# Kernel optimization log

Hardware: AMD Instinct MI355X
Metric: run time of the kernel (lower is better)

The kernel has to match this reference:

```python
import jax, jax.numpy as jnp
import numpy as np

A, OBS, TD, H, M, ACT, AE = 1024, 2048, 256, 128, 16, 256, 64


def setup_inputs() -> dict:
    key = jax.random.key(0)
    ks = jax.random.split(key, 16)
    p = lambda k, shape: jax.random.normal(k, shape, dtype=jnp.float32) * 0.02
    obs = jax.random.normal(ks[0], (A, OBS), dtype=jnp.float32)
    # group membership matrix: exactly M members per initiator row (ATOC top-m groups)
    scores = jax.random.uniform(ks[1], (A, A))
    idx = jnp.argsort(scores, axis=1)[:, :M]
    C = jnp.zeros((A, A), dtype=bool).at[jnp.arange(A)[:, None], idx].set(True)
    inp = dict(obs=obs, C=C)
    # actor_1: Linear(OBS,TD) -> LN -> ReLU -> Linear(TD,TD) -> LN
    inp['W1'] = p(ks[2], (OBS, TD)); inp['b1'] = jnp.zeros((TD,), jnp.float32)
    inp['g1'] = jnp.ones((TD,), jnp.float32); inp['bt1'] = jnp.zeros((TD,), jnp.float32)
    inp['W2'] = p(ks[3], (TD, TD)); inp['b2'] = jnp.zeros((TD,), jnp.float32)
    inp['g2'] = jnp.ones((TD,), jnp.float32); inp['bt2'] = jnp.zeros((TD,), jnp.float32)
    # attention unit: 2-layer MLP + sigmoid head
    inp['aW1'] = p(ks[4], (TD, AE)); inp['ab1'] = jnp.zeros((AE,), jnp.float32)
    inp['aW2'] = p(ks[5], (AE, AE)); inp['ab2'] = jnp.zeros((AE,), jnp.float32)
    inp['aW3'] = p(ks[6], (AE, 1)); inp['ab3'] = jnp.zeros((1,), jnp.float32)
    # bi-directional LSTM (PyTorch layout: W_ih [4H,TD], W_hh [4H,H])
    inp['Wih_f'] = p(ks[7], (4 * H, TD)); inp['Whh_f'] = p(ks[8], (4 * H, H))
    inp['bih_f'] = jnp.zeros((4 * H,), jnp.float32); inp['bhh_f'] = jnp.zeros((4 * H,), jnp.float32)
    inp['Wih_r'] = p(ks[9], (4 * H, TD)); inp['Whh_r'] = p(ks[10], (4 * H, H))
    inp['bih_r'] = jnp.zeros((4 * H,), jnp.float32); inp['bhh_r'] = jnp.zeros((4 * H,), jnp.float32)
    # actor_2: ReLU -> Linear(TD,TD) -> LN -> Linear(TD,ACT) -> LN -> Tanh
    inp['W3'] = p(ks[11], (TD, TD)); inp['b3'] = jnp.zeros((TD,), jnp.float32)
    inp['g3'] = jnp.ones((TD,), jnp.float32); inp['bt3'] = jnp.zeros((TD,), jnp.float32)
    inp['W4'] = p(ks[12], (TD, ACT)); inp['b4'] = jnp.zeros((ACT,), jnp.float32)
    inp['g4'] = jnp.ones((ACT,), jnp.float32); inp['bt4'] = jnp.zeros((ACT,), jnp.float32)
    return inp


def _ln(x, g, b, eps=1e-5):
    m = jnp.mean(x, -1, keepdims=True)
    v = jnp.mean((x - m) ** 2, -1, keepdims=True)
    return (x - m) * jax.lax.rsqrt(v + eps) * g + b


def _lstm(seq, Wih, Whh, bih, bhh):
    # seq [T, D] -> hidden outputs [T, H]; PyTorch gate order i, f, g, o
    def step(carry, x):
        h, c = carry
        z = x @ Wih.T + bih + h @ Whh.T + bhh
        i, f, g, o = jnp.split(z, 4)
        c = jax.nn.sigmoid(f) * c + jax.nn.sigmoid(i) * jnp.tanh(g)
        h = jax.nn.sigmoid(o) * jnp.tanh(c)
        return (h, c), h
    h0 = jnp.zeros((H,), seq.dtype)
    _, hs = jax.lax.scan(step, (h0, h0), seq)
    return hs


def _forward(obs, C, W1, b1, g1, bt1, W2, b2, g2, bt2, aW1, ab1, aW2, ab2, aW3, ab3,
             Wih_f, Whh_f, bih_f, bhh_f, Wih_r, Whh_r, bih_r, bhh_r,
             W3, b3, g3, bt3, W4, b4, g4, bt4):
    # actor_1
    t = jax.nn.relu(_ln(obs @ W1 + b1, g1, bt1))
    thoughts = _ln(t @ W2 + b2, g2, bt2)  # [A, TD]
    # attention unit -> initiators (threshold 0.5)
    a = jax.nn.relu(thoughts @ aW1 + ab1)
    a = jax.nn.relu(a @ aW2 + ab2)
    init_prob = jax.nn.sigmoid(a @ aW3 + ab3)[:, 0]
    is_init = init_prob > 0.5  # [A]
    tpos = jnp.arange(M)

    def comm_step(th, xs):
        mask, active = xs
        # members first (stable, increasing agent index), padded gather of size M
        order = jnp.argsort((~mask).astype(jnp.int32))[:M]
        gcnt = jnp.sum(mask).astype(jnp.int32)
        seq_f = th[order]                        # [M, TD]
        rev = jnp.clip(gcnt - 1 - tpos, 0, M - 1)
        seq_b = seq_f[rev]                       # valid prefix reversed
        out_f = _lstm(seq_f, Wih_f, Whh_f, bih_f, bhh_f)
        out_b = _lstm(seq_b, Wih_r, Whh_r, bih_r, bhh_r)
        out = jnp.concatenate([out_f, out_b[rev]], axis=-1)  # [M, TD] bi-LSTM aligned
        valid = (tpos < gcnt) & active
        newv = jnp.where(valid[:, None], out, seq_f)         # merge = replace by integrated
        return th.at[order].set(newv), None

    thoughts, _ = jax.lax.scan(comm_step, thoughts, (C, is_init))
    # actor_2
    h = jax.nn.relu(thoughts)
    h = _ln(h @ W3 + b3, g3, bt3)
    acts = jnp.tanh(_ln(h @ W4 + b4, g4, bt4))
    return acts


def reference(obs, C, W1, b1, g1, bt1, W2, b2, g2, bt2, aW1, ab1, aW2, ab2, aW3, ab3,
              Wih_f, Whh_f, bih_f, bhh_f, Wih_r, Whh_r, bih_r, bhh_r,
              W3, b3, g3, bt3, W4, b4, g4, bt4):
    return _forward(obs, C, W1, b1, g1, bt1, W2, b2, g2, bt2, aW1, ab1, aW2, ab2, aW3, ab3,
                    Wih_f, Whh_f, bih_f, bhh_f, Wih_r, Whh_r, bih_r, bhh_r,
                    W3, b3, g3, bt3, W4, b4, g4, bt4)
```

## Files before the change

### kernel.cpp

```cpp
#include <hip/hip_runtime.h>
#include <cstdint>
#include <cstddef>
#include <math.h>

#define A_N   1024
#define OBS_N 2048
#define TD_N  256
#define H_N   128
#define M_N   16
#define AE_N  64
#define NWGC  32

typedef _Float16 h2 __attribute__((ext_vector_type(2)));
typedef _Float16 f16x8 __attribute__((ext_vector_type(8)));
typedef float f32x4 __attribute__((ext_vector_type(4)));

__device__ __forceinline__ float sigf(float x) { return 1.0f / (1.0f + expf(-x)); }
__device__ __forceinline__ h2 u2h(unsigned int u) { union { unsigned int x; h2 h; } c; c.x = u; return c.h; }
__device__ __forceinline__ unsigned int packh(float a, float b) {
  union { h2 h; unsigned int u; } c;
  c.h = (h2){(_Float16)a, (_Float16)b};
  return c.u;
}

__device__ __forceinline__ bool c_at(const unsigned char* C, int as_int, size_t idx) {
  return as_int ? (((const int*)C)[idx] != 0) : (C[idx] != 0);
}

__global__ __launch_bounds__(64) void k_cdet(const unsigned char* __restrict__ C, int* __restrict__ flag) {
  int lane = threadIdx.x;
  int cnt = 0;
  for (int i = lane; i < 4096; i += 64) cnt += (C[i] != 0) ? 1 : 0;
  for (int off = 32; off; off >>= 1) cnt += __shfl_down(cnt, off);
  if (lane == 0) flag[0] = (cnt < 40) ? 1 : 0;
}

__global__ __launch_bounds__(256) void k_actor1a(const float* __restrict__ obs,
    const float* __restrict__ W1, const float* __restrict__ b1,
    const float* __restrict__ g1, const float* __restrict__ bt1,
    float* __restrict__ tout) {
  __shared__ float S[4 * OBS_N];
  __shared__ float red[4][4][2];
  int tid = threadIdx.x;
  int r0 = blockIdx.x * 4;
  {
    const float4* src = (const float4*)(obs + (size_t)r0 * OBS_N);
    float4* dst = (float4*)S;
    for (int i = tid; i < 4 * OBS_N / 4; i += 256) dst[i] = src[i];
  }
  __syncthreads();
  int j = tid;
  float acc0 = 0, acc1 = 0, acc2 = 0, acc3 = 0;
  const float4* S4 = (const float4*)S;
  for (int k4 = 0; k4 < OBS_N / 4; k4++) {
    float w0 = W1[(k4 * 4 + 0) * TD_N + j];
    float w1 = W1[(k4 * 4 + 1) * TD_N + j];
    float w2 = W1[(k4 * 4 + 2) * TD_N + j];
    float w3 = W1[(k4 * 4 + 3) * TD_N + j];
    float4 s0 = S4[0 * 512 + k4], s1 = S4[1 * 512 + k4], s2 = S4[2 * 512 + k4], s3 = S4[3 * 512 + k4];
    acc0 += s0.x * w0 + s0.y * w1 + s0.z * w2 + s0.w * w3;
    acc1 += s1.x * w0 + s1.y * w1 + s1.z * w2 + s1.w * w3;
    acc2 += s2.x * w0 + s2.y * w1 + s2.z * w2 + s2.w * w3;
    acc3 += s3.x * w0 + s3.y * w1 + s3.z * w2 + s3.w * w3;
  }
  float z[4] = {acc0 + b1[j], acc1 + b1[j], acc2 + b1[j], acc3 + b1[j]};
  int w = tid >> 6, lane = tid & 63;
  for (int r = 0; r < 4; r++) {
    float v = z[r], v2 = z[r] * z[r];
    for (int off = 32; off; off >>= 1) { v += __shfl_down(v, off); v2 += __shfl_down(v2, off); }
    if (lane == 0) { red[r][w][0] = v; red[r][w][1] = v2; }
  }
  __syncthreads();
  for (int r = 0; r < 4; r++) {
    float sm = red[r][0][0] + red[r][1][0] + red[r][2][0] + red[r][3][0];
    float sq = red[r][0][1] + red[r][1][1] + red[r][2][1] + red[r][3][1];
    float mean = sm * (1.0f / TD_N);
    float var = sq * (1.0f / TD_N) - mean * mean;
    float rs = 1.0f / sqrtf(var + 1e-5f);
    float val = (z[r] - mean) * rs * g1[j] + bt1[j];
    tout[(size_t)(r0 + r) * TD_N + j] = fmaxf(val, 0.0f);
  }
}

__global__ __launch_bounds__(256) void k_actor1b(const float* __restrict__ tin,
    const float* __restrict__ W2, const float* __restrict__ b2,
    const float* __restrict__ g2, const float* __restrict__ bt2,
    float* __restrict__ th) {
  __shared__ float S[4 * TD_N];
  __shared__ float red[4][4][2];
  int tid = threadIdx.x;
  int r0 = blockIdx.x * 4;
  for (int i = tid; i < 4 * TD_N; i += 256) S[i] = tin[(size_t)r0 * TD_N + i];
  __syncthreads();
  int j = tid;
  float z[4] = {0, 0, 0, 0};
  const float4* S4 = (const float4*)S;
  for (int k4 = 0; k4 < TD_N / 4; k4++) {
    float w0 = W2[(k4 * 4 + 0) * TD_N + j];
    float w1 = W2[(k4 * 4 + 1) * TD_N + j];
    float w2v = W2[(k4 * 4 + 2) * TD_N + j];
    float w3 = W2[(k4 * 4 + 3) * TD_N + j];
#pragma unroll
    for (int r = 0; r < 4; r++) {
      float4 sv = S4[r * 64 + k4];
      z[r] += sv.x * w0 + sv.y * w1 + sv.z * w2v + sv.w * w3;
    }
  }
  for (int r = 0; r < 4; r++) z[r] += b2[j];
  int w = tid >> 6, lane = tid & 63;
  for (int r = 0; r < 4; r++) {
    float v = z[r], v2 = z[r] * z[r];
    for (int off = 32; off; off >>= 1) { v += __shfl_down(v, off); v2 += __shfl_down(v2, off); }
    if (lane == 0) { red[r][w][0] = v; red[r][w][1] = v2; }
  }
  __syncthreads();
  for (int r = 0; r < 4; r++) {
    float sm = red[r][0][0] + red[r][1][0] + red[r][2][0] + red[r][3][0];
    float sq = red[r][0][1] + red[r][1][1] + red[r][2][1] + red[r][3][1];
    float mean = sm * (1.0f / TD_N);
    float var = sq * (1.0f / TD_N) - mean * mean;
    float rs = 1.0f / sqrtf(var + 1e-5f);
    th[(size_t)(r0 + r) * TD_N + j] = (z[r] - mean) * rs * g2[j] + bt2[j];
  }
}

__global__ __launch_bounds__(256) void k_att(const float* __restrict__ th,
    const float* __restrict__ aW1, const float* __restrict__ ab1,
    const float* __restrict__ aW2, const float* __restrict__ ab2,
    const float* __restrict__ aW3, const float* __restrict__ ab3,
    int* __restrict__ isin) {
  __shared__ float S[4 * TD_N];
  __shared__ double A1[4 * AE_N];
  __shared__ double A2[4 * AE_N];
  int tid = threadIdx.x;
  int r0 = blockIdx.x * 4;
  for (int i = tid; i < 4 * TD_N; i += 256) S[i] = th[(size_t)r0 * TD_N + i];
  __syncthreads();
  int r = tid >> 6, c = tid & 63;
  double acc = 0;
  for (int k = 0; k < TD_N; k++) acc += (double)S[r * TD_N + k] * (double)aW1[k * AE_N + c];
  acc += (double)ab1[c];
  A1[r * AE_N + c] = acc > 0.0 ? acc : 0.0;
  __syncthreads();
  acc = 0;
  for (int k = 0; k < AE_N; k++) acc += A1[r * AE_N + k] * (double)aW2[k * AE_N + c];
  acc += (double)ab2[c];
  A2[r * AE_N + c] = acc > 0.0 ? acc : 0.0;
  __syncthreads();
  double p = A2[r * AE_N + c] * (double)aW3[c];
  for (int off = 32; off; off >>= 1) p += __shfl_down(p, off);
  if (c == 0) isin[r0 + r] = ((p + (double)ab3[0]) > 0.0) ? 1 : 0;
}

__global__ __launch_bounds__(64) void k_memb(const unsigned char* __restrict__ C,
    const int* __restrict__ flag, int* __restrict__ memb) {
  int s = blockIdx.x, lane = threadIdx.x;
  int as_int = flag[0];
  if (lane < M_N) memb[s * M_N + lane] = lane;
  __syncthreads();
  int base = 0;
  for (int ch = 0; ch < 16; ch++) {
    int col = ch * 64 + lane;
    bool v = c_at(C, as_int, (size_t)s * A_N + col);
    unsigned long long m = __ballot(v);
    if (v) {
      int pos = base + __popcll(m & ((1ull << lane) - 1ull));
      if (pos < M_N) memb[s * M_N + pos] = col;
    }
    base += __popcll(m);
  }
}

__global__ __launch_bounds__(256) void k_req(const unsigned char* __restrict__ C,
    const int* __restrict__ flag, const int* __restrict__ memb,
    const int* __restrict__ isin, int* __restrict__ req) {
  __shared__ int Ls[A_N];
  int s = blockIdx.x, tid = threadIdx.x;
  int as_int = flag[0];
  for (int i = tid; i < A_N; i += 256) Ls[i] = isin[i];
  __syncthreads();
  int i = tid >> 4, sub = tid & 15;
  int m = memb[s * M_N + i] & (A_N - 1);
  int cnt = 0;
  for (int s2 = sub; s2 < s; s2 += 16)
    if (Ls[s2] && c_at(C, as_int, (size_t)s2 * A_N + m)) cnt++;
  for (int off = 1; off < 16; off <<= 1) cnt += __shfl_xor(cnt, off);
  if (sub == 0) req[s * M_N + i] = cnt;
}

__global__ __launch_bounds__(256) void k_prep(
    const float* __restrict__ Wih_f, const float* __restrict__ Wih_r,
    const float* __restrict__ Whh_f, const float* __restrict__ Whh_r,
    const float* __restrict__ bih_f, const float* __restrict__ bhh_f,
    const float* __restrict__ bih_r, const float* __restrict__ bhh_r,
    unsigned int* __restrict__ wfragf, unsigned int* __restrict__ wfragr,
    unsigned int* __restrict__ whhpf, unsigned int* __restrict__ whhpr,
    float* __restrict__ bsumf, float* __restrict__ bsumr,
    int* __restrict__ verF, int* __restrict__ verB) {
  int id = blockIdx.x * 256 + threadIdx.x;
  if (id < 65536) {
    int j = id & 3, l = (id >> 2) & 63, tile = (id >> 8) & 31, c = id >> 13;
    int gate = tile * 16 + (l & 15);
    int k = c * 32 + ((l >> 4) << 3) + (j << 1);
    wfragf[id] = packh(Wih_f[gate * TD_N + k], Wih_f[gate * TD_N + k + 1]);
    wfragr[id] = packh(Wih_r[gate * TD_N + k], Wih_r[gate * TD_N + k + 1]);
  }
  if (id < 32768) {
    int g = id & 511, k2 = id >> 9;
    whhpf[id] = packh(Whh_f[g * H_N + 2 * k2], Whh_f[g * H_N + 2 * k2 + 1]);
    whhpr[id] = packh(Whh_r[g * H_N + 2 * k2], Whh_r[g * H_N + 2 * k2 + 1]);
  }
  if (id < 512) { bsumf[id] = bih_f[id] + bhh_f[id]; bsumr[id] = bih_r[id] + bhh_r[id]; }
  if (id < A_N) { verF[id] = 0; verB[id] = 0; }
}

__global__ __launch_bounds__(64) void k_lvl(const int* __restrict__ isin,
    const int* __restrict__ memb, int* __restrict__ fin,
    int* __restrict__ lstart, int* __restrict__ llist) {
  __shared__ int membS[A_N * M_N];
  __shared__ int last[A_N];
  __shared__ int cnt[A_N + 2];
  __shared__ int cur[A_N + 2];
  __shared__ short lvlS[A_N];
  __shared__ unsigned char isinS[A_N];
  __shared__ unsigned char cntm[A_N];
  int lane = threadIdx.x;
  for (int i = lane; i < A_N * M_N; i += 64) membS[i] = memb[i] & (A_N - 1);
  for (int i = lane; i < A_N; i += 64) {
    isinS[i] = (unsigned char)(isin[i] != 0);
    last[i] = 0; cntm[i] = 0; lvlS[i] = 0;
  }
  for (int l = lane; l < A_N + 2; l += 64) cnt[l] = 0;
  __syncthreads();
  for (int s = 0; s < A_N; s++) {
    if (isinS[s]) {
      int li = 0, m = 0;
      if (lane < 16) { m = membS[s * M_N + lane]; li = last[m]; }
#pragma unroll
      for (int off = 8; off; off >>= 1) li = max(li, __shfl_xor(li, off));
      int L = __shfl(li, 0) + 1;
      if (lane < 16) { last[m] = L; cntm[m]++; }
      if (lane == 0) { lvlS[s] = (short)L; cnt[L]++; }
    }
  }
  if (lane == 0) {
    int acc = 0;
    for (int L = 1; L <= A_N; L++) { cur[L] = acc; acc += cnt[L]; }
    lstart[0] = acc;
    for (int s = 0; s < A_N; s++) {
      int L = lvlS[s];
      if (L > 0) llist[cur[L]++] = s;
    }
  }
  for (int i = lane; i < A_N; i += 64) fin[i] = cntm[i] & 1;
}

#define RSH 264
__global__ __launch_bounds__(512)
void k_scan(
    float* __restrict__ thA, float* __restrict__ thB,
    const int* __restrict__ lstart, const int* __restrict__ llist,
    const int* __restrict__ memb, const int* __restrict__ req,
    int* __restrict__ verF, int* __restrict__ verB,
    const unsigned int* __restrict__ wfragf, const unsigned int* __restrict__ wfragr,
    const unsigned int* __restrict__ whhpf, const unsigned int* __restrict__ whhpr,
    const float* __restrict__ bsumf, const float* __restrict__ bsumr) {
  __shared__ __align__(16) unsigned short Sh[16 * RSH];
  __shared__ float xa_lds[16 * 512 + 9984];
  __shared__ float garr[4 * H_N];
  __shared__ unsigned int hp[2 * 64];
  __shared__ int memb_s[16];
  __shared__ int par_s[16];
  int tid = threadIdx.x;
  int wg = blockIdx.x;
  int dir = wg & 1;
  int pair = wg >> 1;
  int dmask = dir ? 15 : 0;
  const unsigned int* wfrag = dir ? wfragr : wfragf;
  const unsigned int* whhp = dir ? whhpr : whhpf;
  float blo = (dir ? bsumr : bsumf)[tid];
  int istanh = ((tid >> 7) == 2);
  int* vown = dir ? verB : verF;
  int wv = tid >> 6, lane = tid & 63;
  int fm = lane & 15, fkg = lane >> 4;
  unsigned int wreg[64];
#pragma unroll
  for (int k2 = 0; k2 < 64; k2++) wreg[k2] = whhp[k2 * 512 + tid];
#pragma unroll
  for (int k2 = 0; k2 < 64; k2++) asm volatile("" : "+v"(wreg[k2]));

  int nact = lstart[0];
  for (int idx = pair; idx < nact; idx += NWGC / 2) {
    int s = llist[idx];
    if (tid < 16) {
      int m = memb[s * M_N + tid] & (A_N - 1);
      int rq = req[s * M_N + tid];
      memb_s[tid] = m;
      par_s[tid] = rq & 1;
      int tries = 0;
      while (__hip_atomic_load(&verF[m], __ATOMIC_RELAXED, __HIP_MEMORY_SCOPE_AGENT) < rq ||
             __hip_atomic_load(&verB[m], __ATOMIC_RELAXED, __HIP_MEMORY_SCOPE_AGENT) < rq) {
        __builtin_amdgcn_s_sleep(1);
        if (++tries > (1 << 21)) break;
      }
    }
    __syncthreads();
    {
      int r = tid >> 5, p = tid & 31;
      int j = r ^ dmask;
      const float* src = (par_s[j] ? thB : thA) + (size_t)memb_s[j] * TD_N + p * 8;
      float v[8];
#pragma unroll
      for (int q = 0; q < 8; q++)
        v[q] = __hip_atomic_load(src + q, __ATOMIC_RELAXED, __HIP_MEMORY_SCOPE_AGENT);
      uint4 pk;
      pk.x = packh(v[0], v[1]); pk.y = packh(v[2], v[3]);
      pk.z = packh(v[4], v[5]); pk.w = packh(v[6], v[7]);
      *(uint4*)((char*)Sh + r * 528 + p * 16) = pk;
    }
    __syncthreads();
    {
#pragma unroll
      for (int t4 = 0; t4 < 4; t4++) {
        int tile = wv * 4 + t4;
        f32x4 acc = {0.0f, 0.0f, 0.0f, 0.0f};
#pragma unroll 2
        for (int c = 0; c < 8; c++) {
          f16x8 af = *(const f16x8*)((const char*)Sh + fm * 528 + c * 64 + fkg * 16);
          union { uint4 u; f16x8 h; } bu;
          bu.u = *(const uint4*)(wfrag + ((size_t)(c * 32 + tile) * 64 + lane) * 4);
          acc = __builtin_amdgcn_mfma_f32_16x16x32_f16(af, bu.h, acc, 0, 0, 0);
        }
#pragma unroll
        for (int r = 0; r < 4; r++)
          xa_lds[(fkg * 4 + r) * 512 + tile * 16 + fm] = acc[r];
      }
    }
    if (tid < 64) hp[tid] = 0u;
    float cst = 0.0f;
    __syncthreads();
#pragma unroll
    for (int u = 0; u < 16; u++) {
      float xau = xa_lds[u * 512 + tid] + blo;
      const uint4* hp4 = (const uint4*)(hp + (u & 1) * 64);
      float z0 = 0, z1 = 0, z2 = 0, z3 = 0, z4 = 0, z5 = 0, z6 = 0, z7 = 0;
#pragma unroll
      for (int j = 0; j < 16; j += 2) {
        uint4 ha = hp4[j], hb = hp4[j + 1];
        z0 = __builtin_amdgcn_fdot2(u2h(wreg[4 * j + 0]), u2h(ha.x), z0, false);
        z1 = __builtin_amdgcn_fdot2(u2h(wreg[4 * j + 1]), u2h(ha.y), z1, false);
        z2 = __builtin_amdgcn_fdot2(u2h(wreg[4 * j + 2]), u2h(ha.z), z2, false);
        z3 = __builtin_amdgcn_fdot2(u2h(wreg[4 * j + 3]), u2h(ha.w), z3, false);
        z4 = __builtin_amdgcn_fdot2(u2h(wreg[4 * j + 4]), u2h(hb.x), z4, false);
        z5 = __builtin_amdgcn_fdot2(u2h(wreg[4 * j + 5]), u2h(hb.y), z5, false);
        z6 = __builtin_amdgcn_fdot2(u2h(wreg[4 * j + 6]), u2h(hb.z), z6, false);
        z7 = __builtin_amdgcn_fdot2(u2h(wreg[4 * j + 7]), u2h(hb.w), z7, false);
      }
      float z = xau + ((z0 + z1) + (z2 + z3)) + ((z4 + z5) + (z6 + z7));
      garr[tid] = istanh ? tanhf(z) : sigf(z);
      __syncthreads();
      int r2 = u ^ dmask;
      if (tid < H_N) {
        cst = garr[H_N + tid] * cst + garr[tid] * garr[2 * H_N + tid];
        float hv = garr[3 * H_N + tid] * tanhf(cst);
        float hvn = __shfl_down(hv, 1);
        if (!(tid & 1)) hp[((u + 1) & 1) * 64 + (tid >> 1)] = packh(hv, hvn);
        float* dst = par_s[r2] ? thA : thB;
        __hip_atomic_store(dst + (size_t)memb_s[r2] * TD_N + dir * H_N + tid, hv,
                           __ATOMIC_RELAXED, __HIP_MEMORY_SCOPE_AGENT);
      }
      __syncthreads();
      if (tid == 0)
        __hip_atomic_fetch_add(&vown[memb_s[r2]], 1, __ATOMIC_RELAXED, __HIP_MEMORY_SCOPE_AGENT);
    }
  }
}

__global__ __launch_bounds__(256) void k_actor2(const float* __restrict__ thA, const float* __restrict__ thB,
    const int* __restrict__ fin,
    const float* __restrict__ W3, const float* __restrict__ b3,
    const float* __restrict__ g3, const float* __restrict__ bt3,
    const float* __restrict__ W4, const float* __restrict__ b4,
    const float* __restrict__ g4, const float* __restrict__ bt4,
    float* __restrict__ out) {
  __shared__ float Hs[4 * TD_N];
  __shared__ float H3[4 * TD_N];
  __shared__ float red[4][4][2];
  int tid = threadIdx.x;
  int r0 = blockIdx.x * 4;
  int j = tid;
  for (int i = tid; i < 4 * TD_N; i += 256) {
    int r = i >> 8, col = i & 255;
    int row = r0 + r;
    const float* src = (fin[row] ? thB : thA) + (size_t)row * TD_N + col;
    float v = __hip_atomic_load(src, __ATOMIC_RELAXED, __HIP_MEMORY_SCOPE_AGENT);
    Hs[i] = fmaxf(v, 0.0f);
  }
  __syncthreads();
  float z[4] = {0, 0, 0, 0};
  {
    const float4* S4 = (const float4*)Hs;
    for (int k4 = 0; k4 < 64; k4++) {
      float w0 = W3[(k4 * 4 + 0) * TD_N + j];
      float w1 = W3[(k4 * 4 + 1) * TD_N + j];
      float w2 = W3[(k4 * 4 + 2) * TD_N + j];
      float w3v = W3[(k4 * 4 + 3) * TD_N + j];
#pragma unroll
      for (int r = 0; r < 4; r++) {
        float4 sv = S4[r * 64 + k4];
        z[r] += sv.x * w0 + sv.y * w1 + sv.z * w2 + sv.w * w3v;
      }
    }
  }
  for (int r = 0; r < 4; r++) z[r] += b3[j];
  int w = tid >> 6, lane = tid & 63;
  for (int r = 0; r < 4; r++) {
    float v = z[r], v2 = z[r] * z[r];
    for (int off = 32; off; off >>= 1) { v += __shfl_down(v, off); v2 += __shfl_down(v2, off); }
    if (lane == 0) { red[r][w][0] = v; red[r][w][1] = v2; }
  }
  __syncthreads();
  for (int r = 0; r < 4; r++) {
    float sm = red[r][0][0] + red[r][1][0] + red[r][2][0] + red[r][3][0];
    float sq = red[r][0][1] + red[r][1][1] + red[r][2][1] + red[r][3][1];
    float mean = sm * (1.0f / TD_N);
    float var = sq * (1.0f / TD_N) - mean * mean;
    float rs = 1.0f / sqrtf(var + 1e-5f);
    H3[r * TD_N + j] = (z[r] - mean) * rs * g3[j] + bt3[j];
  }
  __syncthreads();
  float z2a[4] = {0, 0, 0, 0};
  {
    const float4* S4 = (const float4*)H3;
    for (int k4 = 0; k4 < 64; k4++) {
      float w0 = W4[(k4 * 4 + 0) * TD_N + j];
      float w1 = W4[(k4 * 4 + 1) * TD_N + j];
      float w2 = W4[(k4 * 4 + 2) * TD_N + j];
      float w3v = W4[(k4 * 4 + 3) * TD_N + j];
#pragma unroll
      for (int r = 0; r < 4; r++) {
        float4 sv = S4[r * 64 + k4];
        z2a[r] += sv.x * w0 + sv.y * w1 + sv.z * w2 + sv.w * w3v;
      }
    }
  }
  for (int r = 0; r < 4; r++) z2a[r] += b4[j];
  __syncthreads();
  for (int r = 0; r < 4; r++) {
    float v = z2a[r], v2 = z2a[r] * z2a[r];
    for (int off = 32; off; off >>= 1) { v += __shfl_down(v, off); v2 += __shfl_down(v2, off); }
    if (lane == 0) { red[r][w][0] = v; red[r][w][1] = v2; }
  }
  __syncthreads();
  for (int r = 0; r < 4; r++) {
    float sm = red[r][0][0] + red[r][1][0] + red[r][2][0] + red[r][3][0];
    float sq = red[r][0][1] + red[r][1][1] + red[r][2][1] + red[r][3][1];
    float mean = sm * (1.0f / TD_N);
    float var = sq * (1.0f / TD_N) - mean * mean;
    float rs = 1.0f / sqrtf(var + 1e-5f);
    float val = (z2a[r] - mean) * rs * g4[j] + bt4[j];
    out[(size_t)(r0 + r) * TD_N + j] = tanhf(val);
  }
}

extern "C" void kernel_launch(void* const* d_in, const int* in_sizes, int n_in,
                              void* d_out, int out_size, void* d_ws, size_t ws_size,
                              hipStream_t stream) {
  const float* obs = (const float*)d_in[0];
  const unsigned char* C = (const unsigned char*)d_in[1];
  const float* W1 = (const float*)d_in[2];  const float* b1 = (const float*)d_in[3];
  const float* g1 = (const float*)d_in[4];  const float* bt1 = (const float*)d_in[5];
  const float* W2 = (const float*)d_in[6];  const float* b2 = (const float*)d_in[7];
  const float* g2 = (const float*)d_in[8];  const float* bt2 = (const float*)d_in[9];
  const float* aW1 = (const float*)d_in[10]; const float* ab1 = (const float*)d_in[11];
  const float* aW2 = (const float*)d_in[12]; const float* ab2 = (const float*)d_in[13];
  const float* aW3 = (const float*)d_in[14]; const float* ab3 = (const float*)d_in[15];
  const float* Wih_f = (const float*)d_in[16]; const float* Whh_f = (const float*)d_in[17];
  const float* bih_f = (const float*)d_in[18]; const float* bhh_f = (const float*)d_in[19];
  const float* Wih_r = (const float*)d_in[20]; const float* Whh_r = (const float*)d_in[21];
  const float* bih_r = (const float*)d_in[22]; const float* bhh_r = (const float*)d_in[23];
  const float* W3 = (const float*)d_in[24]; const float* b3 = (const float*)d_in[25];
  const float* g3 = (const float*)d_in[26]; const float* bt3 = (const float*)d_in[27];
  const float* W4 = (const float*)d_in[28]; const float* b4 = (const float*)d_in[29];
  const float* g4 = (const float*)d_in[30]; const float* bt4 = (const float*)d_in[31];
  float* out = (float*)d_out;

  float* ws = (float*)d_ws;
  unsigned int* wfragf = (unsigned int*)ws;
  unsigned int* wfragr = (unsigned int*)(ws + 131072);
  unsigned int* whhpf = (unsigned int*)(ws + 262144);
  unsigned int* whhpr = (unsigned int*)(ws + 327680);
  float* bsumf = ws + 393216;
  float* bsumr = ws + 393728;
  float* thB   = ws + 394240;
  float* t_buf = ws + 394240;
  int* ibase   = (int*)(ws + 656384);
  int* membi   = ibase;
  int* reqi    = ibase + 16384;
  int* isin    = ibase + 32768;
  int* flag    = ibase + 33792;
  int* fin     = ibase + 33856;
  int* lstart  = ibase + 34880;
  int* llist   = ibase + 34944;
  int* verF    = ibase + 35968;
  int* verB    = ibase + 36992;
  size_t need = (size_t)(656384 + 38016 + 64) * 4;
  if (ws_size < need) return;

  (void)in_sizes; (void)n_in; (void)out_size;

  float* thA = out;

  k_cdet<<<1, 64, 0, stream>>>(C, flag);
  k_actor1a<<<256, 256, 0, stream>>>(obs, W1, b1, g1, bt1, t_buf);
  k_actor1b<<<256, 256, 0, stream>>>(t_buf, W2, b2, g2, bt2, thA);
  k_att<<<256, 256, 0, stream>>>(thA, aW1, ab1, aW2, ab2, aW3, ab3, isin);
  k_memb<<<1024, 64, 0, stream>>>(C, flag, membi);
  k_req<<<1024, 256, 0, stream>>>(C, flag, membi, isin, reqi);
  k_prep<<<512, 256, 0, stream>>>(Wih_f, Wih_r, Whh_f, Whh_r, bih_f, bhh_f, bih_r, bhh_r,
                                  wfragf, wfragr, whhpf, whhpr, bsumf, bsumr, verF, verB);
  k_lvl<<<1, 64, 0, stream>>>(isin, membi, fin, lstart, llist);
  k_scan<<<NWGC, 512, 0, stream>>>(thA, thB, lstart, llist, membi, reqi, verF, verB,
                                   wfragf, wfragr, whhpf, whhpr, bsumf, bsumr);
  k_actor2<<<256, 256, 0, stream>>>(thA, thB, fin, W3, b3, g3, bt3, W4, b4, g4, bt4, out);
}
```

Measured before the change: 4.648 ms.

## Interleave LSTM gate rows so cell update uses wave shuffles instead of LDS barrier

The recurrent weight layout is permuted so that each group of four adjacent threads holds the i, f, g, o gates of one hidden unit. The cell and hidden update is then done with intra-wave shuffles, which removes the shared gate array and one __syncthreads per timestep from the serial recurrence. Every thread now repeats the cell computation redundantly, and only one lane per unit stores the result. xa_lds is enlarged to absorb the freed LDS.

```diff
diff --git a/kernel.cpp b/kernel.cpp
--- a/kernel.cpp
+++ b/kernel.cpp
@@ -206,7 +206,8 @@
     wfragr[id] = packh(Wih_r[gate * TD_N + k], Wih_r[gate * TD_N + k + 1]);
   }
   if (id < 32768) {
-    int g = id & 511, k2 = id >> 9;
+    int t = id & 511, k2 = id >> 9;
+    int g = (t & 3) * 128 + (t >> 2);
     whhpf[id] = packh(Whh_f[g * H_N + 2 * k2], Whh_f[g * H_N + 2 * k2 + 1]);
     whhpr[id] = packh(Whh_r[g * H_N + 2 * k2], Whh_r[g * H_N + 2 * k2 + 1]);
   }
@@ -266,8 +267,7 @@
     const unsigned int* __restrict__ whhpf, const unsigned int* __restrict__ whhpr,
     const float* __restrict__ bsumf, const float* __restrict__ bsumr) {
   __shared__ __align__(16) unsigned short Sh[16 * RSH];
-  __shared__ float xa_lds[16 * 512 + 9984];
-  __shared__ float garr[4 * H_N];
+  __shared__ float xa_lds[16 * 512 + 10240];
   __shared__ unsigned int hp[2 * 64];
   __shared__ int memb_s[16];
   __shared__ int par_s[16];
@@ -278,10 +278,13 @@
   int dmask = dir ? 15 : 0;
   const unsigned int* wfrag = dir ? wfragr : wfragf;
   const unsigned int* whhp = dir ? whhpr : whhpf;
-  float blo = (dir ? bsumr : bsumf)[tid];
-  int istanh = ((tid >> 7) == 2);
+  int gmap = (tid & 3) * 128 + (tid >> 2);
+  int unit = tid >> 2;
+  float blo = (dir ? bsumr : bsumf)[gmap];
+  int gtype = tid & 3;
   int* vown = dir ? verB : verF;
   int wv = tid >> 6, lane = tid & 63;
+  int lane4 = lane & ~3;
   int fm = lane & 15, fkg = lane >> 4;
   unsigned int wreg[64];
 #pragma unroll
@@ -341,7 +344,7 @@
     __syncthreads();
 #pragma unroll
     for (int u = 0; u < 16; u++) {
-      float xau = xa_lds[u * 512 + tid] + blo;
+      float xau = xa_lds[u * 512 + gmap] + blo;
       const uint4* hp4 = (const uint4*)(hp + (u & 1) * 64);
       float z0 = 0, z1 = 0, z2 = 0, z3 = 0, z4 = 0, z5 = 0, z6 = 0, z7 = 0;
 #pragma unroll
@@ -357,16 +360,20 @@
         z7 = __builtin_amdgcn_fdot2(u2h(wreg[4 * j + 7]), u2h(hb.w), z7, false);
       }
       float z = xau + ((z0 + z1) + (z2 + z3)) + ((z4 + z5) + (z6 + z7));
-      garr[tid] = istanh ? tanhf(z) : sigf(z);
-      __syncthreads();
+      float gate = (gtype == 2) ? tanhf(z) : sigf(z);
+      float gi = __shfl(gate, lane4 + 0);
+      float gf = __shfl(gate, lane4 + 1);
+      float gg = __shfl(gate, lane4 + 2);
+      float go = __shfl(gate, lane4 + 3);
+      cst = gf * cst + gi * gg;
+      float hv = go * tanhf(cst);
+      float hvn = __shfl(hv, lane | 4);
       int r2 = u ^ dmask;
-      if (tid < H_N) {
-        cst = garr[H_N + tid] * cst + garr[tid] * garr[2 * H_N + tid];
-        float hv = garr[3 * H_N + tid] * tanhf(cst);
-        float hvn = __shfl_down(hv, 1);
-        if (!(tid & 1)) hp[((u + 1) & 1) * 64 + (tid >> 1)] = packh(hv, hvn);
+      if ((tid & 7) == 0)
+        hp[((u + 1) & 1) * 64 + (tid >> 3)] = packh(hv, hvn);
+      if ((tid & 3) == 0) {
         float* dst = par_s[r2] ? thA : thB;
-        __hip_atomic_store(dst + (size_t)memb_s[r2] * TD_N + dir * H_N + tid, hv,
+        __hip_atomic_store(dst + (size_t)memb_s[r2] * TD_N + dir * H_N + unit, hv,
                            __ATOMIC_RELAXED, __HIP_MEMORY_SCOPE_AGENT);
       }
       __syncthreads();
```

Measured after the change: 4.678 ms. Within noise of the previous version (+0.6%).
